# Kernel optimization log

Measured on AMD Instinct MI355X. Metric: run time of the kernel, lower is better.

The kernel has to match this reference:

```python
import jax, jax.numpy as jnp
import numpy as np

N, E, C = 20000, 320000, 10000
IN, H, D = 768, 8, 64
HD = H * D
SA_H = 128


def _gat(feat, src, dst, W, al, ar, b):
    # DGL GATConv: fc -> per-node attn terms -> edge leaky_relu -> edge softmax over dst -> scatter-add -> bias -> elu
    h = (feat @ W).reshape(N, H, D)                       # [N,H,D]
    el = (h * al).sum(-1)                                 # [N,H]
    er = (h * ar).sum(-1)                                 # [N,H]
    e = jax.nn.leaky_relu(el[src] + er[dst], 0.2)         # [E,H]
    m = jax.ops.segment_max(e, dst, num_segments=N)       # [N,H]
    m = jnp.where(jnp.isfinite(m), m, 0.0)                # zero in-degree nodes
    ee = jnp.exp(e - m[dst])                              # [E,H]
    denom = jax.ops.segment_sum(ee, dst, num_segments=N)  # [N,H]
    a = ee / jnp.maximum(denom[dst], 1e-9)                # [E,H]
    out = jax.ops.segment_sum(a[:, :, None] * h[src], dst, num_segments=N)  # [N,H,D]
    return jax.nn.elu(out + b.reshape(1, H, D))


def _sem(z, w1, b1, w2):
    # SemanticAttention: per-metapath score -> softmax over metapaths -> weighted sum
    w = (jnp.tanh(z @ w1 + b1) @ w2).mean(0)              # [M,1]
    beta = jax.nn.softmax(w, axis=0)                      # [M,1]
    return (beta[None] * z).sum(1)                        # [C,HD]


def setup_inputs():
    key = jax.random.key(0)
    ks = jax.random.split(key, 32)
    inp = {}
    for i in range(3):
        inp[f"feat{i}"] = jax.random.normal(ks[i], (N, IN), jnp.float32)
        inp[f"src{i}"] = jax.random.randint(ks[3 + i], (E,), 0, N, dtype=jnp.int32)
        inp[f"dst{i}"] = jax.random.randint(ks[6 + i], (E,), 0, N, dtype=jnp.int32)
        inp[f"char{i}"] = jnp.arange(C, dtype=jnp.int32)
        inp[f"W{i}"] = jax.random.normal(ks[9 + i], (IN, HD), jnp.float32) * 0.05
        inp[f"al{i}"] = jax.random.normal(ks[12 + i], (H, D), jnp.float32) * 0.05
        inp[f"ar{i}"] = jax.random.normal(ks[15 + i], (H, D), jnp.float32) * 0.05
        inp[f"b{i}"] = jnp.zeros((HD,), jnp.float32)
    inp["sw1"] = jax.random.normal(ks[18], (HD, SA_H), jnp.float32) * 0.05
    inp["sb1"] = jnp.zeros((SA_H,), jnp.float32)
    inp["sw2"] = jax.random.normal(ks[19], (SA_H, 1), jnp.float32) * 0.05
    inp["aw1"] = jax.random.normal(ks[20], (HD, SA_H), jnp.float32) * 0.05
    inp["ab1"] = jnp.zeros((SA_H,), jnp.float32)
    inp["aw2"] = jax.random.normal(ks[21], (SA_H, 1), jnp.float32) * 0.05
    return inp


def reference(feat0, feat1, feat2, src0, src1, src2, dst0, dst1, dst2, char0, char1, char2,
              W0, W1, W2, al0, al1, al2, ar0, ar1, ar2, b0, b1, b2,
              sw1, sb1, sw2, aw1, ab1, aw2):
    h1 = _gat(feat0, src0, dst0, W0, al0, ar0, b0)        # [N,H,D]
    hh = _gat(feat2, src2, dst2, W2, al2, ar2, b2)        # [N,H,D]
    z = jnp.stack([h1[char0].reshape(C, HD), hh[char2].reshape(C, HD)], axis=1)  # [C,2,HD]
    sound = _sem(z, sw1, sb1, sw2)                        # [C,HD]
    h2 = _gat(feat1, src1, dst1, W1, al1, ar1, b1)        # [N,H,D]
    z2 = jnp.stack([sound, h2[char1].reshape(C, HD)], axis=1)  # [C,2,HD]
    sem_emb = _sem(z2, aw1, ab1, aw2).reshape(C, H, D)    # [C,H,D]
    h1 = h1.at[char0].set(sem_emb)
    h2 = h2.at[char1].set(sem_emb)
    hh = hh.at[char2].set(sem_emb)
    return sem_emb, h1.mean(1), h2.mean(1), hh.mean(1)
```

## Files before the change

### kernel.cpp

```cpp
#include <hip/hip_runtime.h>
#include <math.h>

#define NN 20000
#define NE 320000
#define CC 10000
#define KIN 768
#define NH 8
#define ND 64
#define NHD 512
#define NSA 128
#define NBKT 79

#define WTB_SZ (NHD * KIN)
#define W1TB_SZ (NSA * NHD)
#define APAD 136

typedef __attribute__((ext_vector_type(4))) float f32x4;
typedef __attribute__((ext_vector_type(8))) short s16x8;

__device__ __forceinline__ unsigned short f2bf(float f) {
  unsigned u = __float_as_uint(f);
  u += 0x7fffu + ((u >> 16) & 1u);
  return (unsigned short)(u >> 16);
}
__device__ __forceinline__ float bf2f(unsigned short s) {
  return __uint_as_float(((unsigned)s) << 16);
}
__device__ __forceinline__ float bflo(unsigned u) { return __uint_as_float(u << 16); }
__device__ __forceinline__ float bfhi(unsigned u) { return __uint_as_float(u & 0xffff0000u); }

__device__ __forceinline__ void gl_lds16(const void* g, void* l) {
  __builtin_amdgcn_global_load_lds(
      (const __attribute__((address_space(1))) unsigned int*)g,
      (__attribute__((address_space(3))) unsigned int*)l, 16, 0, 0);
}

__global__ void k_prep(const float* __restrict__ W0, const float* __restrict__ W1,
                       const float* __restrict__ W2, const float* __restrict__ sw1,
                       const float* __restrict__ aw1, unsigned short* __restrict__ wtb3,
                       unsigned short* __restrict__ w1tb2, int* __restrict__ deg3,
                       float* __restrict__ scal) {
  int i = blockIdx.x * 256 + threadIdx.x;
  if (i < 3 * WTB_SZ) {
    int g = i / WTB_SZ;
    int j = i - g * WTB_SZ;
    int n = j / KIN, k = j - n * KIN;
    const float* W = (g == 0) ? W0 : (g == 1) ? W1 : W2;
    wtb3[i] = f2bf(W[(size_t)k * NHD + n]);
    return;
  }
  i -= 3 * WTB_SZ;
  if (i < 2 * W1TB_SZ) {
    int p = i / W1TB_SZ;
    int j = i - p * W1TB_SZ;
    int n = j / NHD, k = j - n * NHD;
    const float* W = p ? aw1 : sw1;
    w1tb2[p * W1TB_SZ + n * NHD + k] = f2bf(W[(size_t)k * NSA + n]);
    return;
  }
  i -= 2 * W1TB_SZ;
  if (i < 3 * NN) { deg3[i] = 0; return; }
  i -= 3 * NN;
  if (i < 4) scal[i] = 0.f;
}

__global__ __launch_bounds__(256, 2) void k_gemm_gat(const float* __restrict__ A,
                                                     const unsigned short* __restrict__ Bt,
                                                     unsigned short* __restrict__ outb,
                                                     const float* __restrict__ al,
                                                     const float* __restrict__ ar,
                                                     float* __restrict__ el,
                                                     float* __restrict__ er) {
  __shared__ unsigned short As[64 * APAD];
  __shared__ unsigned short Bs[128 * 128];
  const int bid = blockIdx.x;
  const int xcd = bid & 7, t = bid >> 3;
  const int rowblk = (t >> 2) * 8 + xcd;
  if (rowblk * 64 >= NN) return;
  const int row0 = rowblk * 64;
  const int col0 = (t & 3) * 128;
  const int tid = threadIdx.x;
  const int wv = tid >> 6, lane = tid & 63;
  const int wr = (wv & 1) * 32, wc = (wv >> 1) * 64;

  f32x4 acc[2][4] = {};

  const int l15 = lane & 15;
  const int q = lane >> 4;

  const int arow = tid >> 2, ci = tid & 3;
  int aga = row0 + arow; if (aga > NN - 1) aga = NN - 1;
  const float* ap = A + (size_t)aga * KIN;

  const int binrow = lane >> 4, bch = lane & 15;

  for (int k0 = 0; k0 < KIN; k0 += 128) {
#pragma unroll
    for (int j = 0; j < 8; j++) {
      int rb0 = (wv * 8 + j) * 4;
      int grow = col0 + rb0 + binrow;
      int srcch = bch ^ ((j & 3) * 4 + binrow);
      gl_lds16(Bt + (size_t)grow * KIN + k0 + srcch * 8, Bs + rb0 * 128);
    }
#pragma unroll
    for (int sc = 0; sc < 4; sc++) {
      int s = ci + sc * 4;
      const float* sp = ap + k0 + s * 8;
      float4 f0 = ((const float4*)sp)[0];
      float4 f1 = ((const float4*)sp)[1];
      uint4 pk;
      pk.x = ((unsigned)f2bf(f0.y) << 16) | f2bf(f0.x);
      pk.y = ((unsigned)f2bf(f0.w) << 16) | f2bf(f0.z);
      pk.z = ((unsigned)f2bf(f1.y) << 16) | f2bf(f1.x);
      pk.w = ((unsigned)f2bf(f1.w) << 16) | f2bf(f1.z);
      *(uint4*)(As + arow * APAD + s * 8) = pk;
    }
    __syncthreads();
#pragma unroll
    for (int kk = 0; kk < 4; kk++) {
      s16x8 af[2], bf4[4];
#pragma unroll
      for (int m = 0; m < 2; m++) {
        int r = wr + m * 16 + l15;
        af[m] = *(const s16x8*)(As + r * APAD + (kk * 4 + q) * 8);
      }
#pragma unroll
      for (int n = 0; n < 4; n++) {
        int rB = wc + n * 16 + l15;
        int slot = (kk * 4 + q) ^ l15;
        bf4[n] = *(const s16x8*)(Bs + rB * 128 + slot * 8);
      }
#pragma unroll
      for (int m = 0; m < 2; m++)
#pragma unroll
        for (int n = 0; n < 4; n++)
          acc[m][n] = __builtin_amdgcn_mfma_f32_16x16x32_bf16(af[m], bf4[n], acc[m][n], 0, 0, 0);
    }
    __syncthreads();
  }

  const int cbase = col0 + wc + l15;
  const int rq = (lane >> 4) * 4;
  const int hd = (col0 + wc) >> 6;
  float alc[4], arc[4];
#pragma unroll
  for (int n = 0; n < 4; n++) { alc[n] = al[cbase + n * 16]; arc[n] = ar[cbase + n * 16]; }

#pragma unroll
  for (int m = 0; m < 2; m++) {
#pragma unroll
    for (int r = 0; r < 4; r++) {
      int grow = row0 + wr + m * 16 + rq + r;
      float a = 0.f, b = 0.f;
#pragma unroll
      for (int n = 0; n < 4; n++) {
        float v = acc[m][n][r];
        a += v * alc[n];
        b += v * arc[n];
      }
      a += __shfl_xor(a, 1, 64); a += __shfl_xor(a, 2, 64);
      a += __shfl_xor(a, 4, 64); a += __shfl_xor(a, 8, 64);
      b += __shfl_xor(b, 1, 64); b += __shfl_xor(b, 2, 64);
      b += __shfl_xor(b, 4, 64); b += __shfl_xor(b, 8, 64);
      if (grow < NN) {
        unsigned short* dp = outb + (size_t)grow * NHD + cbase;
#pragma unroll
        for (int n = 0; n < 4; n++) dp[n * 16] = f2bf(acc[m][n][r]);
        if (l15 == 0) {
          el[(size_t)grow * NH + hd] = a;
          er[(size_t)grow * NH + hd] = b;
        }
      }
    }
  }
}

__global__ __launch_bounds__(256, 2) void k_gemm_sem(const unsigned short* __restrict__ A0,
                                                     const unsigned short* __restrict__ A1,
                                                     const unsigned short* __restrict__ Bt,
                                                     const float* __restrict__ b1,
                                                     const float* __restrict__ w2,
                                                     float* __restrict__ scal) {
  __shared__ unsigned short As[128 * 32];
  __shared__ unsigned short Bs[128 * 32];
  __shared__ float rsum[2][128];
  __shared__ float pp[2][2];
  const int M = 2 * CC;
  const int tid = threadIdx.x;
  const int wv = tid >> 6, lane = tid & 63;
  const int row0 = blockIdx.x * 128;
  const int wr = (wv >> 1) * 64, wc = (wv & 1) * 64;
  const int ci = lane & 3, rsub = lane >> 2;

  f32x4 acc[4][4] = {};

  const int l15 = lane & 15;
  const int pc = (((lane >> 4) ^ ((l15 >> 1) & 3))) * 8;

  for (int k0 = 0; k0 < NHD; k0 += 32) {
#pragma unroll
    for (int i = 0; i < 2; i++) {
      int lrow = (wv * 2 + i) * 16 + rsub;
      int kc = (ci ^ ((lrow >> 1) & 3)) << 3;
      int ga = row0 + lrow; if (ga > M - 1) ga = M - 1;
      const unsigned short* Ap = (ga < CC) ? A0 + (size_t)ga * NHD
                                           : A1 + (size_t)(ga - CC) * NHD;
      gl_lds16(Ap + k0 + kc, As + (wv * 2 + i) * 512);
      int gb = lrow;
      gl_lds16(Bt + (size_t)gb * NHD + k0 + kc, Bs + (wv * 2 + i) * 512);
    }
    __syncthreads();
    s16x8 af[4], bf[4];
#pragma unroll
    for (int m = 0; m < 4; m++) {
      af[m] = *(const s16x8*)(As + (wr + m * 16 + l15) * 32 + pc);
      bf[m] = *(const s16x8*)(Bs + (wc + m * 16 + l15) * 32 + pc);
    }
#pragma unroll
    for (int m = 0; m < 4; m++)
#pragma unroll
      for (int n = 0; n < 4; n++)
        acc[m][n] = __builtin_amdgcn_mfma_f32_16x16x32_bf16(af[m], bf[n], acc[m][n], 0, 0, 0);
    __syncthreads();
  }

  if (tid < 128) { rsum[0][tid] = 0.f; rsum[1][tid] = 0.f; }
  __syncthreads();
  const int cb = wc + l15;
  const int rq = (lane >> 4) * 4;
  float b1c[4], w2c[4];
#pragma unroll
  for (int n = 0; n < 4; n++) { b1c[n] = b1[cb + n * 16]; w2c[n] = w2[cb + n * 16]; }
#pragma unroll
  for (int m = 0; m < 4; m++) {
#pragma unroll
    for (int r = 0; r < 4; r++) {
      int rl = wr + m * 16 + rq + r;
      float s = 0.f;
#pragma unroll
      for (int n = 0; n < 4; n++) s += tanhf(acc[m][n][r] + b1c[n]) * w2c[n];
      s += __shfl_xor(s, 1, 64); s += __shfl_xor(s, 2, 64);
      s += __shfl_xor(s, 4, 64); s += __shfl_xor(s, 8, 64);
      if (l15 == 0 && row0 + rl < M) rsum[wv & 1][rl] = s;
    }
  }
  __syncthreads();
  if (tid < 128) {
    int grow = row0 + tid;
    float v = rsum[0][tid] + rsum[1][tid];
    float vA = (grow < CC) ? v : 0.f;
    float vB = (grow >= CC && grow < M) ? v : 0.f;
#pragma unroll
    for (int off = 32; off > 0; off >>= 1) {
      vA += __shfl_xor(vA, off, 64);
      vB += __shfl_xor(vB, off, 64);
    }
    if ((tid & 63) == 0) { pp[tid >> 6][0] = vA; pp[tid >> 6][1] = vB; }
  }
  __syncthreads();
  if (tid == 0) {
    atomicAdd(scal + 0, pp[0][0] + pp[1][0]);
    atomicAdd(scal + 1, pp[0][1] + pp[1][1]);
  }
}

__global__ void k_hist3(const int* __restrict__ d0, const int* __restrict__ d1,
                        const int* __restrict__ d2, int* __restrict__ deg3) {
  int e = blockIdx.x * 256 + threadIdx.x;
  int g = blockIdx.y;
  const int* dst = (g == 0) ? d0 : (g == 1) ? d1 : d2;
  atomicAdd(deg3 + g * NN + dst[e], 1);
}

__global__ __launch_bounds__(1024) void k_scan3(const int* __restrict__ deg3,
                                                int* __restrict__ rowptr3,
                                                int* __restrict__ curB) {
  __shared__ int part[1024];
  const int g = blockIdx.x;
  const int* deg = deg3 + g * NN;
  int* rowptr = rowptr3 + g * (NN + 1);
  int tid = threadIdx.x;
  const int CH = 20;
  int base = tid * CH;
  int s = 0;
  for (int i = 0; i < CH; i++) { int idx = base + i; if (idx < NN) s += deg[idx]; }
  part[tid] = s;
  __syncthreads();
  for (int off = 1; off < 1024; off <<= 1) {
    int u = (tid >= off) ? part[tid - off] : 0;
    int v = part[tid];
    __syncthreads();
    part[tid] = u + v;
    __syncthreads();
  }
  int run = (tid == 0) ? 0 : part[tid - 1];
  for (int i = 0; i < CH; i++) {
    int idx = base + i;
    if (idx < NN) {
      rowptr[idx] = run;
      if ((idx & 255) == 0) curB[g * (NBKT + 1) + (idx >> 8)] = run;
      run += deg[idx];
    }
  }
  if (tid == 1023) rowptr[NN] = part[1023];
}

__global__ __launch_bounds__(1024) void k_coarse(const int* __restrict__ s0,
                                                 const int* __restrict__ s1,
                                                 const int* __restrict__ s2,
                                                 const int* __restrict__ d0,
                                                 const int* __restrict__ d1,
                                                 const int* __restrict__ d2,
                                                 int* __restrict__ curB,
                                                 unsigned* __restrict__ staging) {
  __shared__ int bcnt[NBKT];
  __shared__ int bbase[NBKT];
  int g = blockIdx.y;
  const int* src = (g == 0) ? s0 : (g == 1) ? s1 : s2;
  const int* dst = (g == 0) ? d0 : (g == 1) ? d1 : d2;
  int tid = threadIdx.x;
  if (tid < NBKT) bcnt[tid] = 0;
  __syncthreads();
  int e = blockIdx.x * 1024 + tid;
  bool val = e < NE;
  int b = 0, r = 0, sv = 0, dv = 0;
  if (val) {
    dv = dst[e]; sv = src[e];
    b = dv >> 8;
    r = atomicAdd(&bcnt[b], 1);
  }
  __syncthreads();
  if (tid < NBKT && bcnt[tid] > 0) bbase[tid] = atomicAdd(&curB[g * (NBKT + 1) + tid], bcnt[tid]);
  __syncthreads();
  if (val) staging[(size_t)g * NE + bbase[b] + r] = ((unsigned)sv << 8) | (unsigned)(dv & 255);
}

__global__ __launch_bounds__(1024) void k_fine(const int* __restrict__ rowptr3,
                                               const unsigned* __restrict__ staging,
                                               unsigned short* __restrict__ srcord3) {
  __shared__ int cur[256];
  int g = blockIdx.y, b = blockIdx.x;
  const int* rowptr = rowptr3 + g * (NN + 1);
  int n0 = b << 8;
  int tid = threadIdx.x;
  if (tid < 256) {
    int node = n0 + tid;
    cur[tid] = (node < NN) ? rowptr[node] : 0;
  }
  __syncthreads();
  int nend = n0 + 256; if (nend > NN) nend = NN;
  int start = rowptr[n0];
  int endp = rowptr[nend];
  for (int i = start + tid; i < endp; i += 1024) {
    unsigned u = staging[(size_t)g * NE + i];
    int nl = u & 255;
    int pos = atomicAdd(&cur[nl], 1);
    srcord3[(size_t)g * NE + pos] = (unsigned short)(u >> 8);
  }
}

__global__ __launch_bounds__(256) void k_aggf(const int* __restrict__ rowptr,
                                              const unsigned short* __restrict__ srcord,
                                              const float* __restrict__ el,
                                              const float* __restrict__ er,
                                              const unsigned short* __restrict__ hb,
                                              const float* __restrict__ bias,
                                              unsigned short* __restrict__ ob) {
  __shared__ float aS[4][64 * 8];
  __shared__ int sS[4][64];
  int wv = threadIdx.x >> 6;
  int t = (blockIdx.x * 256 + threadIdx.x) >> 6;
  int lane = threadIdx.x & 63;
  int h = lane >> 3;
  int beg = rowptr[t], end = rowptr[t + 1];

  float4 er0 = ((const float4*)(er + (size_t)t * NH))[0];
  float4 er1 = ((const float4*)(er + (size_t)t * NH))[1];
  float erow[8] = {er0.x, er0.y, er0.z, er0.w, er1.x, er1.y, er1.z, er1.w};

  float acc[8] = {0.f, 0.f, 0.f, 0.f, 0.f, 0.f, 0.f, 0.f};
  float den = 0.f;

  for (int cbeg = beg; cbeg < end; cbeg += 64) {
    int cnt = end - cbeg; if (cnt > 64) cnt = 64;
    bool valid = lane < cnt;
    int pidx = cbeg + lane; if (pidx > end - 1) pidx = end - 1;
    int s = srcord[pidx];
    if (valid) {
      sS[wv][lane] = s;
      float4 a0 = ((const float4*)(el + (size_t)s * NH))[0];
      float4 a1 = ((const float4*)(el + (size_t)s * NH))[1];
      float v[8] = {a0.x + erow[0], a0.y + erow[1], a0.z + erow[2], a0.w + erow[3],
                    a1.x + erow[4], a1.y + erow[5], a1.z + erow[6], a1.w + erow[7]};
#pragma unroll
      for (int k = 0; k < 8; k++) {
        float x = v[k];
        x = x >= 0.f ? x : 0.2f * x;
        aS[wv][lane * 8 + k] = __expf(x);
      }
    }
    const unsigned short* hbl = hb + lane * 8;
    int q = 0;
    for (; q + 3 < cnt; q += 4) {
      int s0 = sS[wv][q], s1 = sS[wv][q + 1], s2 = sS[wv][q + 2], s3 = sS[wv][q + 3];
      float w0 = aS[wv][q * 8 + h];
      float w1 = aS[wv][(q + 1) * 8 + h];
      float w2 = aS[wv][(q + 2) * 8 + h];
      float w3 = aS[wv][(q + 3) * 8 + h];
      uint4 v0 = *(const uint4*)(hbl + (size_t)s0 * NHD);
      uint4 v1 = *(const uint4*)(hbl + (size_t)s1 * NHD);
      uint4 v2 = *(const uint4*)(hbl + (size_t)s2 * NHD);
      uint4 v3 = *(const uint4*)(hbl + (size_t)s3 * NHD);
      den += (w0 + w1) + (w2 + w3);
      acc[0] += w0 * bflo(v0.x); acc[1] += w0 * bfhi(v0.x);
      acc[2] += w0 * bflo(v0.y); acc[3] += w0 * bfhi(v0.y);
      acc[4] += w0 * bflo(v0.z); acc[5] += w0 * bfhi(v0.z);
      acc[6] += w0 * bflo(v0.w); acc[7] += w0 * bfhi(v0.w);
      acc[0] += w1 * bflo(v1.x); acc[1] += w1 * bfhi(v1.x);
      acc[2] += w1 * bflo(v1.y); acc[3] += w1 * bfhi(v1.y);
      acc[4] += w1 * bflo(v1.z); acc[5] += w1 * bfhi(v1.z);
      acc[6] += w1 * bflo(v1.w); acc[7] += w1 * bfhi(v1.w);
      acc[0] += w2 * bflo(v2.x); acc[1] += w2 * bfhi(v2.x);
      acc[2] += w2 * bflo(v2.y); acc[3] += w2 * bfhi(v2.y);
      acc[4] += w2 * bflo(v2.z); acc[5] += w2 * bfhi(v2.z);
      acc[6] += w2 * bflo(v2.w); acc[7] += w2 * bfhi(v2.w);
      acc[0] += w3 * bflo(v3.x); acc[1] += w3 * bfhi(v3.x);
      acc[2] += w3 * bflo(v3.y); acc[3] += w3 * bfhi(v3.y);
      acc[4] += w3 * bflo(v3.z); acc[5] += w3 * bfhi(v3.z);
      acc[6] += w3 * bflo(v3.w); acc[7] += w3 * bfhi(v3.w);
    }
    for (; q < cnt; q++) {
      int s0 = sS[wv][q];
      float w0 = aS[wv][q * 8 + h];
      uint4 v0 = *(const uint4*)(hbl + (size_t)s0 * NHD);
      den += w0;
      acc[0] += w0 * bflo(v0.x); acc[1] += w0 * bfhi(v0.x);
      acc[2] += w0 * bflo(v0.y); acc[3] += w0 * bfhi(v0.y);
      acc[4] += w0 * bflo(v0.z); acc[5] += w0 * bfhi(v0.z);
      acc[6] += w0 * bflo(v0.w); acc[7] += w0 * bfhi(v0.w);
    }
  }

  float dn = 1.f / fmaxf(den, 1e-9f);
  float4 b0 = ((const float4*)(bias + lane * 8))[0];
  float4 b1 = ((const float4*)(bias + lane * 8))[1];
  float r[8];
  r[0] = acc[0] * dn + b0.x; r[1] = acc[1] * dn + b0.y;
  r[2] = acc[2] * dn + b0.z; r[3] = acc[3] * dn + b0.w;
  r[4] = acc[4] * dn + b1.x; r[5] = acc[5] * dn + b1.y;
  r[6] = acc[6] * dn + b1.z; r[7] = acc[7] * dn + b1.w;
#pragma unroll
  for (int j = 0; j < 8; j++) r[j] = r[j] > 0.f ? r[j] : expm1f(r[j]);
  uint4 z;
  z.x = ((unsigned)f2bf(r[1]) << 16) | f2bf(r[0]);
  z.y = ((unsigned)f2bf(r[3]) << 16) | f2bf(r[2]);
  z.z = ((unsigned)f2bf(r[5]) << 16) | f2bf(r[4]);
  z.w = ((unsigned)f2bf(r[7]) << 16) | f2bf(r[6]);
  *(uint4*)(ob + (size_t)t * NHD + lane * 8) = z;
}

__global__ void k_combine_s1(const float* __restrict__ scal,
                             const unsigned short* __restrict__ zA,
                             const unsigned short* __restrict__ zB,
                             unsigned short* __restrict__ outb) {
  int i = blockIdx.x * 256 + threadIdx.x;
  float w0 = scal[0] * (1.f / CC), w1v = scal[1] * (1.f / CC);
  float mx = fmaxf(w0, w1v);
  float e0 = expf(w0 - mx), e1 = expf(w1v - mx);
  float inv = 1.f / (e0 + e1);
  float b0 = e0 * inv, b1v = e1 * inv;
  ushort4 a = ((const ushort4*)zA)[i];
  ushort4 b = ((const ushort4*)zB)[i];
  ushort4 z;
  z.x = f2bf(b0 * bf2f(a.x) + b1v * bf2f(b.x));
  z.y = f2bf(b0 * bf2f(a.y) + b1v * bf2f(b.y));
  z.z = f2bf(b0 * bf2f(a.z) + b1v * bf2f(b.z));
  z.w = f2bf(b0 * bf2f(a.w) + b1v * bf2f(b.w));
  ((ushort4*)outb)[i] = z;
}

__global__ void k_comb2_means(const float* __restrict__ scal,
                              const unsigned short* __restrict__ zsound,
                              const unsigned short* __restrict__ ob0,
                              const unsigned short* __restrict__ ob1,
                              const unsigned short* __restrict__ ob2,
                              float* __restrict__ outf,
                              float* __restrict__ m1, float* __restrict__ m2,
                              float* __restrict__ m3) {
  int idx = blockIdx.x * 256 + threadIdx.x;
  int n = idx >> 6, d = idx & 63;
  if (n < CC) {
    float w0 = scal[0] * (1.f / CC), w1v = scal[1] * (1.f / CC);
    float mx = fmaxf(w0, w1v);
    float e0 = expf(w0 - mx), e1 = expf(w1v - mx);
    float inv = 1.f / (e0 + e1);
    float b0 = e0 * inv, b1v = e1 * inv;
    const unsigned short* zs = zsound + (size_t)n * NHD + d;
    const unsigned short* p1 = ob1 + (size_t)n * NHD + d;
    float* po = outf + (size_t)n * NHD + d;
    float v = 0.f;
#pragma unroll
    for (int h = 0; h < 8; h++) {
      float r = b0 * bf2f(zs[h * 64]) + b1v * bf2f(p1[h * 64]);
      po[h * 64] = r;
      v += r;
    }
    v *= 0.125f;
    m1[idx] = v; m2[idx] = v; m3[idx] = v;
  } else {
    const unsigned short* p0 = ob0 + (size_t)n * NHD + d;
    const unsigned short* p1 = ob1 + (size_t)n * NHD + d;
    const unsigned short* p2 = ob2 + (size_t)n * NHD + d;
    float v0 = 0.f, v1 = 0.f, v2 = 0.f;
#pragma unroll
    for (int h = 0; h < 8; h++) {
      v0 += bf2f(p0[h * 64]); v1 += bf2f(p1[h * 64]); v2 += bf2f(p2[h * 64]);
    }
    m1[idx] = v0 * 0.125f; m2[idx] = v1 * 0.125f; m3[idx] = v2 * 0.125f;
  }
}

extern "C" void kernel_launch(void* const* d_in, const int* in_sizes, int n_in,
                              void* d_out, int out_size, void* d_ws, size_t ws_size,
                              hipStream_t stream) {
  (void)in_sizes; (void)n_in; (void)out_size; (void)ws_size;

  const float* feat[3]; const int* srcp[3]; const int* dstp[3];
  const float* Wp[3]; const float* alp[3]; const float* arp[3]; const float* bp[3];
  for (int g = 0; g < 3; g++) {
    const int base = g * 8;
    feat[g] = (const float*)d_in[base + 0];
    srcp[g] = (const int*)d_in[base + 1];
    dstp[g] = (const int*)d_in[base + 2];
    Wp[g]   = (const float*)d_in[base + 4];
    alp[g]  = (const float*)d_in[base + 5];
    arp[g]  = (const float*)d_in[base + 6];
    bp[g]   = (const float*)d_in[base + 7];
  }
  const float* sw1 = (const float*)d_in[24];
  const float* sb1 = (const float*)d_in[25];
  const float* sw2 = (const float*)d_in[26];
  const float* aw1 = (const float*)d_in[27];
  const float* ab1 = (const float*)d_in[28];
  const float* aw2 = (const float*)d_in[29];

  char* wsp = (char*)d_ws;
  auto alloc = [&](size_t bytes) {
    char* p = wsp;
    wsp += (bytes + 255) & ~(size_t)255;
    return p;
  };
  unsigned short* ob0 = (unsigned short*)alloc((size_t)NN * NHD * 2);
  unsigned short* ob1 = (unsigned short*)alloc((size_t)NN * NHD * 2);
  unsigned short* ob2 = (unsigned short*)alloc((size_t)NN * NHD * 2);
  unsigned short* hb = (unsigned short*)alloc((size_t)NN * NHD * 2);
  unsigned short* wtb3 = (unsigned short*)alloc((size_t)3 * WTB_SZ * 2);
  unsigned short* w1tb2 = (unsigned short*)alloc((size_t)2 * W1TB_SZ * 2);
  unsigned short* sound = (unsigned short*)alloc((size_t)CC * NHD * 2);
  float* el = (float*)alloc((size_t)NN * NH * 4);
  float* er = (float*)alloc((size_t)NN * NH * 4);
  float* scal = (float*)alloc(256);
  int* deg3 = (int*)alloc((size_t)3 * NN * 4);
  int* rowptr3 = (int*)alloc((size_t)3 * (NN + 1) * 4 + 64);
  int* curB = (int*)alloc((size_t)3 * (NBKT + 1) * 4);
  unsigned* staging = (unsigned*)alloc((size_t)3 * NE * 4);
  unsigned short* srcord3 = (unsigned short*)alloc((size_t)3 * NE * 2);

  float* outf = (float*)d_out;
  float* outm1 = outf + (size_t)CC * NHD;
  float* outm2 = outm1 + (size_t)NN * ND;
  float* outm3 = outm2 + (size_t)NN * ND;

  const int PREP_T = 3 * WTB_SZ + 2 * W1TB_SZ + 3 * NN + 4;
  k_prep<<<(PREP_T + 255) / 256, 256, 0, stream>>>(Wp[0], Wp[1], Wp[2], sw1, aw1,
                                                   wtb3, w1tb2, deg3, scal);
  k_hist3<<<dim3(NE / 256, 3), 256, 0, stream>>>(dstp[0], dstp[1], dstp[2], deg3);
  k_scan3<<<3, 1024, 0, stream>>>(deg3, rowptr3, curB);
  k_coarse<<<dim3((NE + 1023) / 1024, 3), 1024, 0, stream>>>(
      srcp[0], srcp[1], srcp[2], dstp[0], dstp[1], dstp[2], curB, staging);
  k_fine<<<dim3(NBKT, 3), 1024, 0, stream>>>(rowptr3, staging, srcord3);

  auto gat = [&](int g, unsigned short* ob) {
    k_gemm_gat<<<1280, 256, 0, stream>>>(
        feat[g], wtb3 + (size_t)g * WTB_SZ, hb, alp[g], arp[g], el, er);
    k_aggf<<<NN * 64 / 256, 256, 0, stream>>>(rowptr3 + g * (NN + 1), srcord3 + (size_t)g * NE,
                                              el, er, hb, bp[g], ob);
  };

  gat(0, ob0);
  gat(2, ob2);

  k_gemm_sem<<<(2 * CC + 127) / 128, 256, 0, stream>>>(ob0, ob2, w1tb2, sb1, sw2, scal);
  k_combine_s1<<<CC * NHD / 4 / 256, 256, 0, stream>>>(scal, ob0, ob2, sound);

  gat(1, ob1);

  k_gemm_sem<<<(2 * CC + 127) / 128, 256, 0, stream>>>(sound, ob1, w1tb2 + W1TB_SZ, ab1, aw2, scal + 2);
  k_comb2_means<<<NN * 64 / 256, 256, 0, stream>>>(scal + 2, sound, ob0, ob1, ob2,
                                                   outf, outm1, outm2, outm3);
}
```

Before: 423.3 us.

## Batch all three GAT projections and aggregations into single launches

The three per-metapath GEMM and aggregation kernels, previously launched one graph at a time, are merged into one GEMM launch over 3x the blocks and one aggregation launch with a grid y-dimension selecting the graph. Per-graph hb/el/er buffers replace the single shared scratch so the graphs no longer serialize on it. This cuts launch count and tail effects and fills the GPU better, at the cost of three times the intermediate workspace and a larger working set in cache.

```diff
diff --git a/kernel.cpp b/kernel.cpp
--- a/kernel.cpp
+++ b/kernel.cpp
@@ -14,6 +14,7 @@
 #define WTB_SZ (NHD * KIN)
 #define W1TB_SZ (NSA * NHD)
 #define APAD 136
+#define GB 1280
 
 typedef __attribute__((ext_vector_type(4))) float f32x4;
 typedef __attribute__((ext_vector_type(8))) short s16x8;
@@ -64,19 +65,28 @@
   if (i < 4) scal[i] = 0.f;
 }
 
-__global__ __launch_bounds__(256, 2) void k_gemm_gat(const float* __restrict__ A,
-                                                     const unsigned short* __restrict__ Bt,
-                                                     unsigned short* __restrict__ outb,
-                                                     const float* __restrict__ al,
-                                                     const float* __restrict__ ar,
-                                                     float* __restrict__ el,
-                                                     float* __restrict__ er) {
+__global__ __launch_bounds__(256, 2) void k_gemm_gat3(
+    const float* __restrict__ f0, const float* __restrict__ f1, const float* __restrict__ f2,
+    const unsigned short* __restrict__ wtb3, unsigned short* __restrict__ hb3,
+    const float* __restrict__ al0, const float* __restrict__ al1, const float* __restrict__ al2,
+    const float* __restrict__ ar0, const float* __restrict__ ar1, const float* __restrict__ ar2,
+    float* __restrict__ el3, float* __restrict__ er3) {
   __shared__ unsigned short As[64 * APAD];
   __shared__ unsigned short Bs[128 * 128];
-  const int bid = blockIdx.x;
-  const int xcd = bid & 7, t = bid >> 3;
+  const int bidg = blockIdx.x;
+  const int g = bidg / GB;
+  const int bid = bidg - g * GB;
+  const int xcd = bidg & 7, t = bid >> 3;
   const int rowblk = (t >> 2) * 8 + xcd;
   if (rowblk * 64 >= NN) return;
+  const float* A = (g == 0) ? f0 : (g == 1) ? f1 : f2;
+  const float* al = (g == 0) ? al0 : (g == 1) ? al1 : al2;
+  const float* ar = (g == 0) ? ar0 : (g == 1) ? ar1 : ar2;
+  const unsigned short* Bt = wtb3 + (size_t)g * WTB_SZ;
+  unsigned short* outb = hb3 + (size_t)g * NN * NHD;
+  float* el = el3 + (size_t)g * NN * NH;
+  float* er = er3 + (size_t)g * NN * NH;
+
   const int row0 = rowblk * 64;
   const int col0 = (t & 3) * 128;
   const int tid = threadIdx.x;
@@ -106,13 +116,13 @@
     for (int sc = 0; sc < 4; sc++) {
       int s = ci + sc * 4;
       const float* sp = ap + k0 + s * 8;
-      float4 f0 = ((const float4*)sp)[0];
-      float4 f1 = ((const float4*)sp)[1];
+      float4 fa = ((const float4*)sp)[0];
+      float4 fb = ((const float4*)sp)[1];
       uint4 pk;
-      pk.x = ((unsigned)f2bf(f0.y) << 16) | f2bf(f0.x);
-      pk.y = ((unsigned)f2bf(f0.w) << 16) | f2bf(f0.z);
-      pk.z = ((unsigned)f2bf(f1.y) << 16) | f2bf(f1.x);
-      pk.w = ((unsigned)f2bf(f1.w) << 16) | f2bf(f1.z);
+      pk.x = ((unsigned)f2bf(fa.y) << 16) | f2bf(fa.x);
+      pk.y = ((unsigned)f2bf(fa.w) << 16) | f2bf(fa.z);
+      pk.z = ((unsigned)f2bf(fb.y) << 16) | f2bf(fb.x);
+      pk.w = ((unsigned)f2bf(fb.w) << 16) | f2bf(fb.z);
       *(uint4*)(As + arow * APAD + s * 8) = pk;
     }
     __syncthreads();
@@ -359,15 +369,26 @@
   }
 }
 
-__global__ __launch_bounds__(256) void k_aggf(const int* __restrict__ rowptr,
-                                              const unsigned short* __restrict__ srcord,
-                                              const float* __restrict__ el,
-                                              const float* __restrict__ er,
-                                              const unsigned short* __restrict__ hb,
-                                              const float* __restrict__ bias,
-                                              unsigned short* __restrict__ ob) {
+__global__ __launch_bounds__(256) void k_aggf3(const int* __restrict__ rowptr3,
+                                               const unsigned short* __restrict__ srcord3,
+                                               const float* __restrict__ el3,
+                                               const float* __restrict__ er3,
+                                               const unsigned short* __restrict__ hb3,
+                                               const float* __restrict__ b0p,
+                                               const float* __restrict__ b1p,
+                                               const float* __restrict__ b2p,
+                                               unsigned short* __restrict__ ob3) {
   __shared__ float aS[4][64 * 8];
   __shared__ int sS[4][64];
+  int g = blockIdx.y;
+  const int* rowptr = rowptr3 + g * (NN + 1);
+  const unsigned short* srcord = srcord3 + (size_t)g * NE;
+  const float* el = el3 + (size_t)g * NN * NH;
+  const float* er = er3 + (size_t)g * NN * NH;
+  const unsigned short* hb = hb3 + (size_t)g * NN * NHD;
+  const float* bias = (g == 0) ? b0p : (g == 1) ? b1p : b2p;
+  unsigned short* ob = ob3 + (size_t)g * NN * NHD;
+
   int wv = threadIdx.x >> 6;
   int t = (blockIdx.x * 256 + threadIdx.x) >> 6;
   int lane = threadIdx.x & 63;
@@ -550,21 +571,23 @@
     wsp += (bytes + 255) & ~(size_t)255;
     return p;
   };
-  unsigned short* ob0 = (unsigned short*)alloc((size_t)NN * NHD * 2);
-  unsigned short* ob1 = (unsigned short*)alloc((size_t)NN * NHD * 2);
-  unsigned short* ob2 = (unsigned short*)alloc((size_t)NN * NHD * 2);
-  unsigned short* hb = (unsigned short*)alloc((size_t)NN * NHD * 2);
+  unsigned short* ob3 = (unsigned short*)alloc((size_t)3 * NN * NHD * 2);
+  unsigned short* hb3 = (unsigned short*)alloc((size_t)3 * NN * NHD * 2);
   unsigned short* wtb3 = (unsigned short*)alloc((size_t)3 * WTB_SZ * 2);
   unsigned short* w1tb2 = (unsigned short*)alloc((size_t)2 * W1TB_SZ * 2);
   unsigned short* sound = (unsigned short*)alloc((size_t)CC * NHD * 2);
-  float* el = (float*)alloc((size_t)NN * NH * 4);
-  float* er = (float*)alloc((size_t)NN * NH * 4);
+  float* el3 = (float*)alloc((size_t)3 * NN * NH * 4);
+  float* er3 = (float*)alloc((size_t)3 * NN * NH * 4);
   float* scal = (float*)alloc(256);
   int* deg3 = (int*)alloc((size_t)3 * NN * 4);
   int* rowptr3 = (int*)alloc((size_t)3 * (NN + 1) * 4 + 64);
   int* curB = (int*)alloc((size_t)3 * (NBKT + 1) * 4);
   unsigned* staging = (unsigned*)alloc((size_t)3 * NE * 4);
   unsigned short* srcord3 = (unsigned short*)alloc((size_t)3 * NE * 2);
+
+  unsigned short* ob0 = ob3;
+  unsigned short* ob1 = ob3 + (size_t)NN * NHD;
+  unsigned short* ob2 = ob3 + (size_t)2 * NN * NHD;
 
   float* outf = (float*)d_out;
   float* outm1 = outf + (size_t)CC * NHD;
@@ -580,20 +603,14 @@
       srcp[0], srcp[1], srcp[2], dstp[0], dstp[1], dstp[2], curB, staging);
   k_fine<<<dim3(NBKT, 3), 1024, 0, stream>>>(rowptr3, staging, srcord3);
 
-  auto gat = [&](int g, unsigned short* ob) {
-    k_gemm_gat<<<1280, 256, 0, stream>>>(
-        feat[g], wtb3 + (size_t)g * WTB_SZ, hb, alp[g], arp[g], el, er);
-    k_aggf<<<NN * 64 / 256, 256, 0, stream>>>(rowptr3 + g * (NN + 1), srcord3 + (size_t)g * NE,
-                                              el, er, hb, bp[g], ob);
-  };
-
-  gat(0, ob0);
-  gat(2, ob2);
+  k_gemm_gat3<<<3 * GB, 256, 0, stream>>>(feat[0], feat[1], feat[2], wtb3, hb3,
+                                          alp[0], alp[1], alp[2], arp[0], arp[1], arp[2],
+                                          el3, er3);
+  k_aggf3<<<dim3(NN * 64 / 256, 3), 256, 0, stream>>>(rowptr3, srcord3, el3, er3, hb3,
+                                                      bp[0], bp[1], bp[2], ob3);
 
   k_gemm_sem<<<(2 * CC + 127) / 128, 256, 0, stream>>>(ob0, ob2, w1tb2, sb1, sw2, scal);
   k_combine_s1<<<CC * NHD / 4 / 256, 256, 0, stream>>>(scal, ob0, ob2, sound);
-
-  gat(1, ob1);
 
   k_gemm_sem<<<(2 * CC + 127) / 128, 256, 0, stream>>>(sound, ob1, w1tb2 + W1TB_SZ, ab1, aw2, scal + 2);
   k_comb2_means<<<NN * 64 / 256, 256, 0, stream>>>(scal + 2, sound, ob0, ob1, ob2,
```

Result: faster. 411.0 us (-2.9%).
